# Performance work log

Hardware: AMD Instinct MI355X
Metric: run time of the kernel (lower is better)

Reference implementation:

```python
import jax, jax.numpy as jnp
import numpy as np

B, M, D, H, FF = 2, 2048, 1024, 16, 2624
DH = D // H  # 64, power of 2 as required by the kernel
EPS = 1e-5
THETA = 10000.0


def setup_inputs() -> dict:
    key = jax.random.key(0)
    ks = jax.random.split(key, 12)
    hidden_states = jax.random.normal(ks[0], (B, M, D), dtype=jnp.float32)
    # padding mask: 1=valid, 0=pad; vary valid lengths per batch element
    lengths = jnp.array([M, 3 * M // 4], dtype=jnp.int32)
    attention_mask = (jnp.arange(M)[None, :] < lengths[:, None]).astype(jnp.int32)
    s = 0.02
    return {
        "hidden_states": hidden_states,
        "attention_mask": attention_mask,
        "ln1_w": jnp.ones((D,), jnp.float32),
        "ln1_b": jnp.zeros((D,), jnp.float32),
        "wqkv_w": s * jax.random.normal(ks[1], (3 * D, D), jnp.float32),
        "wqkv_b": jnp.zeros((3 * D,), jnp.float32),
        "wo_w": s * jax.random.normal(ks[2], (D, D), jnp.float32),
        "ln2_w": jnp.ones((D,), jnp.float32),
        "ln2_b": jnp.zeros((D,), jnp.float32),
        "wi_w": s * jax.random.normal(ks[3], (2 * FF, D), jnp.float32),
        "wo_mlp_w": s * jax.random.normal(ks[4], (D, FF), jnp.float32),
    }


def _layernorm(x, w, b):
    mu = jnp.mean(x, axis=-1, keepdims=True)
    var = jnp.mean(jnp.square(x - mu), axis=-1, keepdims=True)
    return (x - mu) * jax.lax.rsqrt(var + EPS) * w + b


def _rope(q, k):
    # q,k: [B,H,M,DH]; half-split RoPE (q1' = q1*c - q2*s; q2' = q1*s + q2*c)
    half = DH // 2
    inv_freq = 1.0 / (THETA ** (jnp.arange(0, DH, 2, dtype=jnp.float32) / DH))  # [half]
    freqs = jnp.arange(M, dtype=jnp.float32)[:, None] * inv_freq[None, :]      # [M, half]
    c = jnp.cos(freqs)[None, None]  # [1,1,M,half]
    s = jnp.sin(freqs)[None, None]
    q1, q2 = q[..., :half], q[..., half:]
    k1, k2 = k[..., :half], k[..., half:]
    q = jnp.concatenate([q1 * c - q2 * s, q1 * s + q2 * c], axis=-1)
    k = jnp.concatenate([k1 * c - k2 * s, k1 * s + k2 * c], axis=-1)
    return q, k


def reference(hidden_states, attention_mask, ln1_w, ln1_b, wqkv_w, wqkv_b,
              wo_w, ln2_w, ln2_b, wi_w, wo_mlp_w):
    x = hidden_states
    xn = _layernorm(x, ln1_w, ln1_b)
    qkv = (xn @ wqkv_w.T + wqkv_b).reshape(B, M, 3, H, DH)
    q, k, v = [jnp.transpose(qkv[:, :, i], (0, 2, 1, 3)) for i in range(3)]  # [B,H,M,DH]
    q, k = _rope(q, k)
    scale = 1.0 / np.sqrt(DH)
    scores = jnp.einsum("bhmd,bhnd->bhmn", q, k) * scale
    keep = (attention_mask > 0)[:, None, None, :]  # [B,1,1,M] key-padding mask
    scores = jnp.where(keep, scores, -jnp.inf)
    attn = jax.nn.softmax(scores, axis=-1)
    o = jnp.einsum("bhmn,bhnd->bhmd", attn, v)
    attn_out = jnp.transpose(o, (0, 2, 1, 3)).reshape(B, M, D)
    x = x + attn_out @ wo_w.T
    # ModernBERT GeGLU MLP
    h = _layernorm(x, ln2_w, ln2_b)
    g = h @ wi_w.T
    inp, gate = g[..., :FF], g[..., FF:]
    x = x + (jax.nn.gelu(inp, approximate=False) * gate) @ wo_mlp_w.T
    return x
```

## Files before the change

### kernel.cpp

```cpp
#include <hip/hip_runtime.h>
#include <hip/hip_bf16.h>
#include <math.h>

#define BB 2
#define MM 2048
#define DD 1024
#define HH 16
#define DHH 64
#define FF_ 2624
#define FFP 2688
#define TT (BB*MM)

typedef unsigned short u16;
typedef __attribute__((ext_vector_type(4))) unsigned short ushort4v;
typedef __attribute__((ext_vector_type(8))) short short8;
typedef __attribute__((ext_vector_type(4))) float floatx4;

#define SCALE2 0.18033688011112043f

__device__ __forceinline__ u16 f2bf(float f) {
    __hip_bfloat16 h = __float2bfloat16(f);
    return *(u16*)&h;
}
__device__ __forceinline__ float bf2f(u16 u) {
    __hip_bfloat16 h; *(u16*)&h = u;
    return __bfloat162float(h);
}
__device__ __forceinline__ float gelu_exact(float x) {
    return 0.5f * x * (1.0f + erff(x * 0.70710678118654752f));
}
__device__ __forceinline__ void gload_lds16(const void* g, void* l) {
    __builtin_amdgcn_global_load_lds(
        (const __attribute__((address_space(1))) unsigned int*)g,
        (__attribute__((address_space(3))) unsigned int*)l, 16, 0, 0);
}

__device__ __forceinline__ int xcd_swizzle(int id, int nb) {
    if (nb & 7) return id;
    return (id & 7) * (nb >> 3) + (id >> 3);
}

__global__ void cvt_all(const float* __restrict__ wqkv, const float* __restrict__ wo,
                        const float* __restrict__ wi, const float* __restrict__ womlp,
                        u16* __restrict__ dqkv, u16* __restrict__ dwo,
                        u16* __restrict__ dinp, u16* __restrict__ dgate,
                        u16* __restrict__ dmlp, float2* __restrict__ tab) {
    int bid = blockIdx.x, tid = threadIdx.x;
    if (bid < 3072) {
        int i = (bid * 256 + tid) * 4;
        float4 v = *(const float4*)(wqkv + i);
        ushort4v o = {f2bf(v.x), f2bf(v.y), f2bf(v.z), f2bf(v.w)};
        *(ushort4v*)(dqkv + i) = o;
    } else if (bid < 4096) {
        int i = ((bid - 3072) * 256 + tid) * 4;
        float4 v = *(const float4*)(wo + i);
        ushort4v o = {f2bf(v.x), f2bf(v.y), f2bf(v.z), f2bf(v.w)};
        *(ushort4v*)(dwo + i) = o;
    } else if (bid < 4096 + 2 * FFP) {
        int seg = (bid - 4096) / FFP;
        int row = (bid - 4096) % FFP;
        u16* dst = seg ? dgate : dinp;
        const float* src = wi + (size_t)(seg ? FF_ : 0) * DD;
        int c = tid * 4;
        ushort4v o = {0, 0, 0, 0};
        if (row < FF_) {
            float4 v = *(const float4*)(src + (size_t)row * DD + c);
            o.x = f2bf(v.x); o.y = f2bf(v.y); o.z = f2bf(v.z); o.w = f2bf(v.w);
        }
        *(ushort4v*)(dst + (size_t)row * DD + c) = o;
    } else if (bid < 4096 + 2 * FFP + 1024) {
        int row = bid - 4096 - 2 * FFP;
        for (int c = tid * 4; c < FFP; c += 1024) {
            ushort4v o = {0, 0, 0, 0};
            if (c < FF_) {
                float4 v = *(const float4*)(womlp + (size_t)row * FF_ + c);
                o.x = f2bf(v.x); o.y = f2bf(v.y); o.z = f2bf(v.z); o.w = f2bf(v.w);
            }
            *(ushort4v*)(dmlp + (size_t)row * FFP + c) = o;
        }
    } else {
        int bq = bid - (4096 + 2 * FFP + 1024);
        int base = bq * 1024;
        for (int idx = tid; idx < 1024; idx += 256) {
            int e = base + idx;
            int mi = e >> 5, i = e & 31;
            float fr = (float)mi * powf(10000.0f, -(float)i / 32.0f);
            tab[e] = make_float2(cosf(fr), sinf(fr));
        }
    }
}

__global__ void ln_kernel(const float* __restrict__ x, const float* __restrict__ w,
                          const float* __restrict__ b, u16* __restrict__ out) {
    int row = blockIdx.x;
    int tid = threadIdx.x;
    const float4 v = ((const float4*)(x + (size_t)row * DD))[tid];
    float s  = v.x + v.y + v.z + v.w;
    float ss = v.x*v.x + v.y*v.y + v.z*v.z + v.w*v.w;
    #pragma unroll
    for (int o = 32; o > 0; o >>= 1) { s += __shfl_down(s, o); ss += __shfl_down(ss, o); }
    __shared__ float sbuf[4], ssbuf[4];
    int wid = tid >> 6;
    if ((tid & 63) == 0) { sbuf[wid] = s; ssbuf[wid] = ss; }
    __syncthreads();
    float st  = sbuf[0] + sbuf[1] + sbuf[2] + sbuf[3];
    float sst = ssbuf[0] + ssbuf[1] + ssbuf[2] + ssbuf[3];
    float mean = st * (1.0f / DD);
    float var  = sst * (1.0f / DD) - mean * mean;
    float rstd = rsqrtf(var + 1e-5f);
    const float4 wv = ((const float4*)w)[tid];
    const float4 bv = ((const float4*)b)[tid];
    ushort4v o;
    o.x = f2bf((v.x - mean) * rstd * wv.x + bv.x);
    o.y = f2bf((v.y - mean) * rstd * wv.y + bv.y);
    o.z = f2bf((v.z - mean) * rstd * wv.z + bv.z);
    o.w = f2bf((v.w - mean) * rstd * wv.w + bv.w);
    ((ushort4v*)(out + (size_t)row * DD))[tid] = o;
}


template<int MODE, bool OUT_BF16>
__global__ __launch_bounds__(256)
void mfma_gemm(const u16* __restrict__ A, const u16* __restrict__ W,
               const float* __restrict__ bias, const void* __restrict__ add,
               void* __restrict__ Cout, int N, int K) {
    __shared__ u16 As[2][128 * 32];
    __shared__ u16 Bs[2][128 * 32];
    int tid = threadIdx.x;
    int w = tid >> 6, lane = tid & 63;
    int q = lane >> 4, m = lane & 15;

    int nbx = gridDim.x;
    int id = xcd_swizzle(blockIdx.y * nbx + blockIdx.x, nbx * gridDim.y);
    int bx = id % nbx, by = id / nbx;
    int row0 = by * 128, col0 = bx * 128;
    int wm = (w >> 1) * 64, wn = (w & 1) * 64;

    floatx4 acc[4][4];
    #pragma unroll
    for (int i = 0; i < 4; i++)
        #pragma unroll
        for (int j = 0; j < 4; j++)
            acc[i][j] = (floatx4){0.f, 0.f, 0.f, 0.f};

    int lrow = lane >> 2;
    int lcg  = (lane & 3) ^ ((lrow >> 1) & 3);
    const u16* Ag = A + (size_t)(row0 + w * 32 + lrow) * K + lcg * 8;
    const u16* Bg = W + (size_t)(col0 + w * 32 + lrow) * K + lcg * 8;
    int NT = K >> 5;
    int slot8 = (q ^ ((m >> 1) & 3)) * 8;

    gload_lds16(Ag,                    &As[0][(w * 32) * 32]);
    gload_lds16(Ag + (size_t)16 * K,   &As[0][(w * 32 + 16) * 32]);
    gload_lds16(Bg,                    &Bs[0][(w * 32) * 32]);
    gload_lds16(Bg + (size_t)16 * K,   &Bs[0][(w * 32 + 16) * 32]);
    __syncthreads();

    for (int t = 0; t < NT; ++t) {
        int cur = t & 1;
        if (t + 1 < NT) {
            const u16* Aq = Ag + (size_t)(t + 1) * 32;
            const u16* Bq = Bg + (size_t)(t + 1) * 32;
            gload_lds16(Aq,                  &As[cur ^ 1][(w * 32) * 32]);
            gload_lds16(Aq + (size_t)16 * K, &As[cur ^ 1][(w * 32 + 16) * 32]);
            gload_lds16(Bq,                  &Bs[cur ^ 1][(w * 32) * 32]);
            gload_lds16(Bq + (size_t)16 * K, &Bs[cur ^ 1][(w * 32 + 16) * 32]);
        }
        short8 af[4], bf[4];
        #pragma unroll
        for (int f = 0; f < 4; f++) {
            af[f] = *(const short8*)&As[cur][(wm + f * 16 + m) * 32 + slot8];
            bf[f] = *(const short8*)&Bs[cur][(wn + f * 16 + m) * 32 + slot8];
        }
        __builtin_amdgcn_s_setprio(1);
        #pragma unroll
        for (int mf = 0; mf < 4; mf++)
            #pragma unroll
            for (int nf = 0; nf < 4; nf++)
                acc[mf][nf] = __builtin_amdgcn_mfma_f32_16x16x32_bf16(
                    af[mf], bf[nf], acc[mf][nf], 0, 0, 0);
        __builtin_amdgcn_s_setprio(0);
        if (t + 1 < NT) __syncthreads();
    }

    #pragma unroll
    for (int nf = 0; nf < 4; nf++) {
        int col = col0 + wn + nf * 16 + m;
        float bv = 0.f;
        if (MODE == 0 && bias) bv = bias[col];
        #pragma unroll
        for (int mf = 0; mf < 4; mf++) {
            #pragma unroll
            for (int r = 0; r < 4; r++) {
                int row = row0 + wm + mf * 16 + q * 4 + r;
                size_t idx = (size_t)row * N + col;
                float vacc = acc[mf][nf][r] + bv;
                if (MODE == 1) vacc += ((const float*)add)[idx];
                if (OUT_BF16) ((u16*)Cout)[idx] = f2bf(vacc);
                else          ((float*)Cout)[idx] = vacc;
            }
        }
    }
}

__global__ __launch_bounds__(256)
void mfma_gemm_qkv(const u16* __restrict__ A, const u16* __restrict__ W,
                   const float* __restrict__ bias, const float2* __restrict__ tab,
                   u16* __restrict__ qb, u16* __restrict__ kb, u16* __restrict__ vtb) {
    __shared__ u16 As[2][128 * 32];
    __shared__ u16 Bs[2][128 * 32];
    int tid = threadIdx.x;
    int w = tid >> 6, lane = tid & 63;
    int q = lane >> 4, m = lane & 15;

    int nbx = gridDim.x;
    int id = xcd_swizzle(blockIdx.y * nbx + blockIdx.x, nbx * gridDim.y);
    int bx = id % nbx, by = id / nbx;
    int row0 = by * 128, col0 = bx * 128;
    int wm = (w >> 1) * 64, wn = (w & 1) * 64;

    floatx4 acc[4][4];
    #pragma unroll
    for (int i = 0; i < 4; i++)
        #pragma unroll
        for (int j = 0; j < 4; j++)
            acc[i][j] = (floatx4){0.f, 0.f, 0.f, 0.f};

    int lrow = lane >> 2;
    int lcg  = (lane & 3) ^ ((lrow >> 1) & 3);
    const u16* Ag = A + (size_t)(row0 + w * 32 + lrow) * DD + lcg * 8;
    const u16* Bg = W + (size_t)(col0 + w * 32 + lrow) * DD + lcg * 8;
    const int NT = DD >> 5;
    int slot8 = (q ^ ((m >> 1) & 3)) * 8;

    gload_lds16(Ag,                     &As[0][(w * 32) * 32]);
    gload_lds16(Ag + (size_t)16 * DD,   &As[0][(w * 32 + 16) * 32]);
    gload_lds16(Bg,                     &Bs[0][(w * 32) * 32]);
    gload_lds16(Bg + (size_t)16 * DD,   &Bs[0][(w * 32 + 16) * 32]);
    __syncthreads();

    for (int t = 0; t < NT; ++t) {
        int cur = t & 1;
        if (t + 1 < NT) {
            const u16* Aq = Ag + (size_t)(t + 1) * 32;
            const u16* Bq = Bg + (size_t)(t + 1) * 32;
            gload_lds16(Aq,                   &As[cur ^ 1][(w * 32) * 32]);
            gload_lds16(Aq + (size_t)16 * DD, &As[cur ^ 1][(w * 32 + 16) * 32]);
            gload_lds16(Bq,                   &Bs[cur ^ 1][(w * 32) * 32]);
            gload_lds16(Bq + (size_t)16 * DD, &Bs[cur ^ 1][(w * 32 + 16) * 32]);
        }
        short8 af[4], bf[4];
        #pragma unroll
        for (int f = 0; f < 4; f++) {
            af[f] = *(const short8*)&As[cur][(wm + f * 16 + m) * 32 + slot8];
            bf[f] = *(const short8*)&Bs[cur][(wn + f * 16 + m) * 32 + slot8];
        }
        __builtin_amdgcn_s_setprio(1);
        #pragma unroll
        for (int mf = 0; mf < 4; mf++)
            #pragma unroll
            for (int nf = 0; nf < 4; nf++)
                acc[mf][nf] = __builtin_amdgcn_mfma_f32_16x16x32_bf16(
                    af[mf], bf[nf], acc[mf][nf], 0, 0, 0);
        __builtin_amdgcn_s_setprio(0);
        if (t + 1 < NT) __syncthreads();
    }

    int wcol = col0 + wn;
    int seg  = wcol >> 6;
    int b    = row0 >> 11;
    int mi0  = (row0 & 2047) + wm;

    float b0[4];
    #pragma unroll
    for (int nf = 0; nf < 4; nf++) b0[nf] = bias[wcol + nf * 16 + m];

    if (seg < 32) {
        int hq = seg & 15;
        u16* dst = (seg < 16 ? qb : kb) + (size_t)(b * HH + hq) * MM * DHH;
        #pragma unroll
        for (int mf = 0; mf < 4; mf++) {
            #pragma unroll
            for (int r = 0; r < 4; r++) {
                int mi = mi0 + mf * 16 + q * 4 + r;
                float2 cs0 = tab[mi * 32 + m];
                float2 cs1 = tab[mi * 32 + 16 + m];
                float a0 = acc[mf][0][r] + b0[0];
                float a1 = acc[mf][1][r] + b0[1];
                float a2 = acc[mf][2][r] + b0[2];
                float a3 = acc[mf][3][r] + b0[3];
                size_t base = (size_t)mi * DHH;
                dst[base + m]      = f2bf(a0 * cs0.x - a2 * cs0.y);
                dst[base + 32 + m] = f2bf(a0 * cs0.y + a2 * cs0.x);
                dst[base + 16 + m] = f2bf(a1 * cs1.x - a3 * cs1.y);
                dst[base + 48 + m] = f2bf(a1 * cs1.y + a3 * cs1.x);
            }
        }
    } else {
        int hv = seg & 15;
        u16* dst = vtb + (size_t)(b * HH + hv) * DHH * MM;
        #pragma unroll
        for (int nf = 0; nf < 4; nf++) {
            int d = nf * 16 + m;
            #pragma unroll
            for (int mf = 0; mf < 4; mf++) {
                int mi = mi0 + mf * 16 + q * 4;
                ushort4v o;
                o.x = f2bf(acc[mf][nf][0] + b0[nf]);
                o.y = f2bf(acc[mf][nf][1] + b0[nf]);
                o.z = f2bf(acc[mf][nf][2] + b0[nf]);
                o.w = f2bf(acc[mf][nf][3] + b0[nf]);
                *(ushort4v*)(dst + (size_t)d * MM + mi) = o;
            }
        }
    }
}

__global__ __launch_bounds__(256, 2)
void mfma_gemm_glu(const u16* __restrict__ A, const u16* __restrict__ W1,
                   const u16* __restrict__ W2, u16* __restrict__ Cout) {
    __shared__ u16 As [2][128 * 32];
    __shared__ u16 B1s[2][128 * 32];
    __shared__ u16 B2s[2][128 * 32];
    int tid = threadIdx.x;
    int w = tid >> 6, lane = tid & 63;
    int q = lane >> 4, m = lane & 15;

    int nbx = gridDim.x;
    int id = xcd_swizzle(blockIdx.y * nbx + blockIdx.x, nbx * gridDim.y);
    int bx = id % nbx, by = id / nbx;
    int row0 = by * 128, col0 = bx * 128;
    int wm = (w >> 1) * 64, wn = (w & 1) * 64;

    floatx4 acc1[4][4], acc2[4][4];
    #pragma unroll
    for (int i = 0; i < 4; i++)
        #pragma unroll
        for (int j = 0; j < 4; j++) {
            acc1[i][j] = (floatx4){0.f, 0.f, 0.f, 0.f};
            acc2[i][j] = (floatx4){0.f, 0.f, 0.f, 0.f};
        }

    int lrow = lane >> 2;
    int lcg  = (lane & 3) ^ ((lrow >> 1) & 3);
    const u16* Ag  = A  + (size_t)(row0 + w * 32 + lrow) * DD + lcg * 8;
    const u16* B1g = W1 + (size_t)(col0 + w * 32 + lrow) * DD + lcg * 8;
    const u16* B2g = W2 + (size_t)(col0 + w * 32 + lrow) * DD + lcg * 8;
    const int NT = DD >> 5;
    int slot8 = (q ^ ((m >> 1) & 3)) * 8;

    gload_lds16(Ag,                    &As [0][(w * 32) * 32]);
    gload_lds16(Ag  + (size_t)16 * DD, &As [0][(w * 32 + 16) * 32]);
    gload_lds16(B1g,                   &B1s[0][(w * 32) * 32]);
    gload_lds16(B1g + (size_t)16 * DD, &B1s[0][(w * 32 + 16) * 32]);
    gload_lds16(B2g,                   &B2s[0][(w * 32) * 32]);
    gload_lds16(B2g + (size_t)16 * DD, &B2s[0][(w * 32 + 16) * 32]);
    __syncthreads();

    for (int t = 0; t < NT; ++t) {
        int cur = t & 1;
        if (t + 1 < NT) {
            const u16* Aq  = Ag  + (size_t)(t + 1) * 32;
            const u16* B1q = B1g + (size_t)(t + 1) * 32;
            const u16* B2q = B2g + (size_t)(t + 1) * 32;
            gload_lds16(Aq,                    &As [cur ^ 1][(w * 32) * 32]);
            gload_lds16(Aq  + (size_t)16 * DD, &As [cur ^ 1][(w * 32 + 16) * 32]);
            gload_lds16(B1q,                   &B1s[cur ^ 1][(w * 32) * 32]);
            gload_lds16(B1q + (size_t)16 * DD, &B1s[cur ^ 1][(w * 32 + 16) * 32]);
            gload_lds16(B2q,                   &B2s[cur ^ 1][(w * 32) * 32]);
            gload_lds16(B2q + (size_t)16 * DD, &B2s[cur ^ 1][(w * 32 + 16) * 32]);
        }
        short8 af[4], b1f[4], b2f[4];
        #pragma unroll
        for (int f = 0; f < 4; f++) {
            af[f]  = *(const short8*)&As [cur][(wm + f * 16 + m) * 32 + slot8];
            b1f[f] = *(const short8*)&B1s[cur][(wn + f * 16 + m) * 32 + slot8];
            b2f[f] = *(const short8*)&B2s[cur][(wn + f * 16 + m) * 32 + slot8];
        }
        __builtin_amdgcn_s_setprio(1);
        #pragma unroll
        for (int mf = 0; mf < 4; mf++)
            #pragma unroll
            for (int nf = 0; nf < 4; nf++) {
                acc1[mf][nf] = __builtin_amdgcn_mfma_f32_16x16x32_bf16(
                    af[mf], b1f[nf], acc1[mf][nf], 0, 0, 0);
                acc2[mf][nf] = __builtin_amdgcn_mfma_f32_16x16x32_bf16(
                    af[mf], b2f[nf], acc2[mf][nf], 0, 0, 0);
            }
        __builtin_amdgcn_s_setprio(0);
        if (t + 1 < NT) __syncthreads();
    }

    #pragma unroll
    for (int nf = 0; nf < 4; nf++) {
        int col = col0 + wn + nf * 16 + m;
        #pragma unroll
        for (int mf = 0; mf < 4; mf++) {
            #pragma unroll
            for (int r = 0; r < 4; r++) {
                int row = row0 + wm + mf * 16 + q * 4 + r;
                Cout[(size_t)row * FFP + col] =
                    f2bf(gelu_exact(acc1[mf][nf][r]) * acc2[mf][nf][r]);
            }
        }
    }
}

__global__ __launch_bounds__(256, 2)
void flash_attn_mfma(const u16* __restrict__ q, const u16* __restrict__ k,
                     const u16* __restrict__ vt, const int* __restrict__ mask,
                     u16* __restrict__ out) {
    __shared__ __align__(16) u16 Ks[64 * 64];
    __shared__ __align__(16) u16 Vt[64 * 64];
    __shared__ __align__(16) u16 QP[128 * 64];

    int tid = threadIdx.x;
    int w = tid >> 6, lane = tid & 63;
    int quad = lane >> 4, m = lane & 15;
    int mt = blockIdx.x, h = blockIdx.y, b = blockIdx.z;
    int m0 = mt * 128;
    size_t bh = (size_t)(b * HH + h);
    const u16* qb  = q  + (bh * MM + m0) * DHH;
    const u16* kb  = k  + bh * MM * DHH;
    const u16* vtb = vt + bh * DHH * MM;

    int lrow = lane >> 3, lcg = (lane & 7) ^ lrow;

    {
        const u16* Qg = qb + (size_t)(w * 32 + lrow) * DHH + lcg * 8;
        u16* Ql = &QP[(w * 32) * 64];
        #pragma unroll
        for (int t = 0; t < 4; t++)
            gload_lds16(Qg + (size_t)(t * 8) * DHH, Ql + t * 8 * 64);
    }
    __syncthreads();

    short8 qf[2][2];
    #pragma unroll
    for (int mf = 0; mf < 2; mf++)
        #pragma unroll
        for (int ks = 0; ks < 2; ks++) {
            int slot = (ks * 4 + quad) ^ (m & 7);
            qf[mf][ks] = *(const short8*)&QP[(w * 32 + mf * 16 + m) * 64 + slot * 8];
        }

    floatx4 O[2][4];
    #pragma unroll
    for (int mf = 0; mf < 2; mf++)
        #pragma unroll
        for (int df = 0; df < 4; df++)
            O[mf][df] = (floatx4){0.f, 0.f, 0.f, 0.f};
    float lsum[2][4] = {};

    u16* Pw = &QP[(w * 32) * 64];

    for (int n0 = 0; n0 < MM; n0 += 64) {
        if (mask[b * MM + n0] == 0) break;
        __syncthreads();

        {
            const u16* Kg = kb + (size_t)(n0 + w * 16 + lrow) * DHH + lcg * 8;
            u16* Kl = &Ks[(w * 16) * 64];
            #pragma unroll
            for (int t = 0; t < 2; t++)
                gload_lds16(Kg + (size_t)(t * 8) * DHH, Kl + t * 8 * 64);
            const u16* Vg = vtb + (size_t)(w * 16 + lrow) * MM + n0 + lcg * 8;
            u16* Vl = &Vt[(w * 16) * 64];
            #pragma unroll
            for (int t = 0; t < 2; t++)
                gload_lds16(Vg + (size_t)(t * 8) * MM, Vl + t * 8 * 64);
        }
        __syncthreads();

        floatx4 S[2][4];
        #pragma unroll
        for (int mf = 0; mf < 2; mf++)
            #pragma unroll
            for (int nf = 0; nf < 4; nf++)
                S[mf][nf] = (floatx4){0.f, 0.f, 0.f, 0.f};
        #pragma unroll
        for (int ks = 0; ks < 2; ks++) {
            short8 kf[4];
            #pragma unroll
            for (int nf = 0; nf < 4; nf++) {
                int slot = (ks * 4 + quad) ^ (m & 7);
                kf[nf] = *(const short8*)&Ks[(nf * 16 + m) * 64 + slot * 8];
            }
            #pragma unroll
            for (int mf = 0; mf < 2; mf++)
                #pragma unroll
                for (int nf = 0; nf < 4; nf++)
                    S[mf][nf] = __builtin_amdgcn_mfma_f32_16x16x32_bf16(
                        qf[mf][ks], kf[nf], S[mf][nf], 0, 0, 0);
        }

        #pragma unroll
        for (int mf = 0; mf < 2; mf++)
            #pragma unroll
            for (int r = 0; r < 4; r++) {
                float s0 = exp2f(S[mf][0][r] * SCALE2);
                float s1 = exp2f(S[mf][1][r] * SCALE2);
                float s2 = exp2f(S[mf][2][r] * SCALE2);
                float s3 = exp2f(S[mf][3][r] * SCALE2);
                S[mf][0][r] = s0; S[mf][1][r] = s1; S[mf][2][r] = s2; S[mf][3][r] = s3;
                lsum[mf][r] += (s0 + s1) + (s2 + s3);
            }

        #pragma unroll
        for (int mf = 0; mf < 2; mf++)
            #pragma unroll
            for (int nf = 0; nf < 4; nf++)
                #pragma unroll
                for (int r = 0; r < 4; r++) {
                    int prow = mf * 16 + quad * 4 + r;
                    int pcol = nf * 16 + m;
                    int slot = (pcol >> 3) ^ (prow & 7);
                    Pw[prow * 64 + slot * 8 + (pcol & 7)] = f2bf(S[mf][nf][r]);
                }

        #pragma unroll
        for (int ks = 0; ks < 2; ks++) {
            short8 pf[2], vf[4];
            #pragma unroll
            for (int mf = 0; mf < 2; mf++) {
                int slot = (ks * 4 + quad) ^ (m & 7);
                pf[mf] = *(const short8*)&Pw[(mf * 16 + m) * 64 + slot * 8];
            }
            #pragma unroll
            for (int df = 0; df < 4; df++) {
                int d = df * 16 + m;
                int slot = (ks * 4 + quad) ^ (d & 7);
                vf[df] = *(const short8*)&Vt[d * 64 + slot * 8];
            }
            #pragma unroll
            for (int mf = 0; mf < 2; mf++)
                #pragma unroll
                for (int df = 0; df < 4; df++)
                    O[mf][df] = __builtin_amdgcn_mfma_f32_16x16x32_bf16(
                        pf[mf], vf[df], O[mf][df], 0, 0, 0);
        }
    }

    #pragma unroll
    for (int mf = 0; mf < 2; mf++) {
        float inv[4];
        #pragma unroll
        for (int r = 0; r < 4; r++) {
            float s = lsum[mf][r];
            #pragma unroll
            for (int o = 1; o < 16; o <<= 1) s += __shfl_xor(s, o);
            inv[r] = 1.0f / s;
        }
        #pragma unroll
        for (int df = 0; df < 4; df++) {
            int d = df * 16 + m;
            #pragma unroll
            for (int r = 0; r < 4; r++) {
                int row = m0 + w * 32 + mf * 16 + quad * 4 + r;
                out[((size_t)(b * MM) + row) * DD + h * DHH + d] =
                    f2bf(O[mf][df][r] * inv[r]);
            }
        }
    }
}

extern "C" void kernel_launch(void* const* d_in, const int* in_sizes, int n_in,
                              void* d_out, int out_size, void* d_ws, size_t ws_size,
                              hipStream_t stream) {
    const float* hidden   = (const float*)d_in[0];
    const int*   mask     = (const int*)d_in[1];
    const float* ln1_w    = (const float*)d_in[2];
    const float* ln1_b    = (const float*)d_in[3];
    const float* wqkv_w   = (const float*)d_in[4];
    const float* wqkv_b   = (const float*)d_in[5];
    const float* wo_w     = (const float*)d_in[6];
    const float* ln2_w    = (const float*)d_in[7];
    const float* ln2_b    = (const float*)d_in[8];
    const float* wi_w     = (const float*)d_in[9];
    const float* wo_mlp_w = (const float*)d_in[10];
    float* out = (float*)d_out;

    char* ws = (char*)d_ws;
    u16* wqkv_bf  = (u16*)(ws);
    u16* wo_bf    = (u16*)(ws + 6291456);
    u16* wi_inp   = (u16*)(ws + 8388608);
    u16* wi_gate  = (u16*)(ws + 13893632);
    u16* womlp_bf = (u16*)(ws + 19398656);
    u16* xn       = (u16*)(ws + 24903680);
    float2* rtab  = (float2*)(ws + 33292288);
    u16* qb       = (u16*)(ws + 58458112);
    u16* kb       = (u16*)(ws + 66846720);
    u16* vtb      = (u16*)(ws + 75235328);
    u16* attn_out = (u16*)(ws + 83623936);
    u16* hb       = (u16*)(ws + 92012544);
    u16* act      = (u16*)(ws + 58458112);

    cvt_all<<<4096 + 2 * FFP + 1024 + 64, 256, 0, stream>>>(
        wqkv_w, wo_w, wi_w, wo_mlp_w, wqkv_bf, wo_bf, wi_inp, wi_gate, womlp_bf, rtab);
    ln_kernel<<<TT, 256, 0, stream>>>(hidden, ln1_w, ln1_b, xn);
    mfma_gemm_qkv<<<dim3(3 * DD / 128, TT / 128), 256, 0, stream>>>(
        xn, wqkv_bf, wqkv_b, rtab, qb, kb, vtb);
    flash_attn_mfma<<<dim3(MM / 128, HH, BB), 256, 0, stream>>>(qb, kb, vtb, mask, attn_out);
    mfma_gemm<1, false><<<dim3(DD / 128, TT / 128), 256, 0, stream>>>(
        attn_out, wo_bf, nullptr, hidden, out, DD, DD);
    ln_kernel<<<TT, 256, 0, stream>>>(out, ln2_w, ln2_b, hb);
    mfma_gemm_glu<<<dim3(FFP / 128, TT / 128), 256, 0, stream>>>(
        hb, wi_inp, wi_gate, act);
    mfma_gemm<1, false><<<dim3(DD / 128, TT / 128), 256, 0, stream>>>(
        act, womlp_bf, nullptr, out, out, DD, FFP);
}
```

Measured before the change: 411.6 us.

## Shrink GEMM tiles to 128x64 and use explicit vmcnt waits with raw barriers

```diff
diff --git a/kernel.cpp b/kernel.cpp
--- a/kernel.cpp
+++ b/kernel.cpp
@@ -17,6 +17,9 @@
 typedef __attribute__((ext_vector_type(4))) float floatx4;
 
 #define SCALE2 0.18033688011112043f
+
+#define WAITVM(N) asm volatile("s_waitcnt vmcnt(" #N ")" ::: "memory")
+#define CFENCE()  asm volatile("" ::: "memory")
 
 __device__ __forceinline__ u16 f2bf(float f) {
     __hip_bfloat16 h = __float2bfloat16(f);
@@ -120,12 +123,12 @@
 
 
 template<int MODE, bool OUT_BF16>
-__global__ __launch_bounds__(256)
-void mfma_gemm(const u16* __restrict__ A, const u16* __restrict__ W,
-               const float* __restrict__ bias, const void* __restrict__ add,
-               void* __restrict__ Cout, int N, int K) {
+__global__ __launch_bounds__(256, 4)
+void mfma_gemm64(const u16* __restrict__ A, const u16* __restrict__ W,
+                 const float* __restrict__ bias, const void* __restrict__ add,
+                 void* __restrict__ Cout, int N, int K) {
     __shared__ u16 As[2][128 * 32];
-    __shared__ u16 Bs[2][128 * 32];
+    __shared__ u16 Bs[2][64 * 32];
     int tid = threadIdx.x;
     int w = tid >> 6, lane = tid & 63;
     int q = lane >> 4, m = lane & 15;
@@ -133,28 +136,26 @@
     int nbx = gridDim.x;
     int id = xcd_swizzle(blockIdx.y * nbx + blockIdx.x, nbx * gridDim.y);
     int bx = id % nbx, by = id / nbx;
-    int row0 = by * 128, col0 = bx * 128;
-    int wm = (w >> 1) * 64, wn = (w & 1) * 64;
-
-    floatx4 acc[4][4];
+    int row0 = by * 128, col0 = bx * 64;
+    int wm = (w >> 1) * 64, wn = (w & 1) * 32;
+
+    floatx4 acc[4][2];
     #pragma unroll
     for (int i = 0; i < 4; i++)
         #pragma unroll
-        for (int j = 0; j < 4; j++)
+        for (int j = 0; j < 2; j++)
             acc[i][j] = (floatx4){0.f, 0.f, 0.f, 0.f};
 
     int lrow = lane >> 2;
     int lcg  = (lane & 3) ^ ((lrow >> 1) & 3);
     const u16* Ag = A + (size_t)(row0 + w * 32 + lrow) * K + lcg * 8;
-    const u16* Bg = W + (size_t)(col0 + w * 32 + lrow) * K + lcg * 8;
+    const u16* Bg = W + (size_t)(col0 + w * 16 + lrow) * K + lcg * 8;
     int NT = K >> 5;
     int slot8 = (q ^ ((m >> 1) & 3)) * 8;
 
-    gload_lds16(Ag,                    &As[0][(w * 32) * 32]);
-    gload_lds16(Ag + (size_t)16 * K,   &As[0][(w * 32 + 16) * 32]);
-    gload_lds16(Bg,                    &Bs[0][(w * 32) * 32]);
-    gload_lds16(Bg + (size_t)16 * K,   &Bs[0][(w * 32 + 16) * 32]);
-    __syncthreads();
+    gload_lds16(Ag,                  &As[0][(w * 32) * 32]);
+    gload_lds16(Ag + (size_t)16 * K, &As[0][(w * 32 + 16) * 32]);
+    gload_lds16(Bg,                  &Bs[0][(w * 16) * 32]);
 
     for (int t = 0; t < NT; ++t) {
         int cur = t & 1;
@@ -163,28 +164,36 @@
             const u16* Bq = Bg + (size_t)(t + 1) * 32;
             gload_lds16(Aq,                  &As[cur ^ 1][(w * 32) * 32]);
             gload_lds16(Aq + (size_t)16 * K, &As[cur ^ 1][(w * 32 + 16) * 32]);
-            gload_lds16(Bq,                  &Bs[cur ^ 1][(w * 32) * 32]);
-            gload_lds16(Bq + (size_t)16 * K, &Bs[cur ^ 1][(w * 32 + 16) * 32]);
-        }
-        short8 af[4], bf[4];
-        #pragma unroll
-        for (int f = 0; f < 4; f++) {
+            gload_lds16(Bq,                  &Bs[cur ^ 1][(w * 16) * 32]);
+            WAITVM(3);
+        } else {
+            WAITVM(0);
+        }
+        __builtin_amdgcn_s_barrier();
+        CFENCE();
+        short8 af[4], bf[2];
+        #pragma unroll
+        for (int f = 0; f < 4; f++)
             af[f] = *(const short8*)&As[cur][(wm + f * 16 + m) * 32 + slot8];
+        #pragma unroll
+        for (int f = 0; f < 2; f++)
             bf[f] = *(const short8*)&Bs[cur][(wn + f * 16 + m) * 32 + slot8];
-        }
         __builtin_amdgcn_s_setprio(1);
         #pragma unroll
         for (int mf = 0; mf < 4; mf++)
             #pragma unroll
-            for (int nf = 0; nf < 4; nf++)
+            for (int nf = 0; nf < 2; nf++)
                 acc[mf][nf] = __builtin_amdgcn_mfma_f32_16x16x32_bf16(
                     af[mf], bf[nf], acc[mf][nf], 0, 0, 0);
         __builtin_amdgcn_s_setprio(0);
-        if (t + 1 < NT) __syncthreads();
-    }
-
-    #pragma unroll
-    for (int nf = 0; nf < 4; nf++) {
+        if (t + 1 < NT) {
+            __builtin_amdgcn_s_barrier();
+            CFENCE();
+        }
+    }
+
+    #pragma unroll
+    for (int nf = 0; nf < 2; nf++) {
         int col = col0 + wn + nf * 16 + m;
         float bv = 0.f;
         if (MODE == 0 && bias) bv = bias[col];
@@ -203,12 +212,12 @@
     }
 }
 
-__global__ __launch_bounds__(256)
+__global__ __launch_bounds__(256, 4)
 void mfma_gemm_qkv(const u16* __restrict__ A, const u16* __restrict__ W,
                    const float* __restrict__ bias, const float2* __restrict__ tab,
                    u16* __restrict__ qb, u16* __restrict__ kb, u16* __restrict__ vtb) {
     __shared__ u16 As[2][128 * 32];
-    __shared__ u16 Bs[2][128 * 32];
+    __shared__ u16 Bs[2][64 * 32];
     int tid = threadIdx.x;
     int w = tid >> 6, lane = tid & 63;
     int q = lane >> 4, m = lane & 15;
@@ -216,12 +225,12 @@
     int nbx = gridDim.x;
     int id = xcd_swizzle(blockIdx.y * nbx + blockIdx.x, nbx * gridDim.y);
     int bx = id % nbx, by = id / nbx;
-    int row0 = by * 128, col0 = bx * 128;
-    int wm = (w >> 1) * 64, wn = (w & 1) * 64;
-
-    floatx4 acc[4][4];
-    #pragma unroll
-    for (int i = 0; i < 4; i++)
+    int row0 = by * 128, col0 = bx * 64;
+    int wm = w * 32;
+
+    floatx4 acc[2][4];
+    #pragma unroll
+    for (int i = 0; i < 2; i++)
         #pragma unroll
         for (int j = 0; j < 4; j++)
             acc[i][j] = (floatx4){0.f, 0.f, 0.f, 0.f};
@@ -229,15 +238,13 @@
     int lrow = lane >> 2;
     int lcg  = (lane & 3) ^ ((lrow >> 1) & 3);
     const u16* Ag = A + (size_t)(row0 + w * 32 + lrow) * DD + lcg * 8;
-    const u16* Bg = W + (size_t)(col0 + w * 32 + lrow) * DD + lcg * 8;
+    const u16* Bg = W + (size_t)(col0 + w * 16 + lrow) * DD + lcg * 8;
     const int NT = DD >> 5;
     int slot8 = (q ^ ((m >> 1) & 3)) * 8;
 
-    gload_lds16(Ag,                     &As[0][(w * 32) * 32]);
-    gload_lds16(Ag + (size_t)16 * DD,   &As[0][(w * 32 + 16) * 32]);
-    gload_lds16(Bg,                     &Bs[0][(w * 32) * 32]);
-    gload_lds16(Bg + (size_t)16 * DD,   &Bs[0][(w * 32 + 16) * 32]);
-    __syncthreads();
+    gload_lds16(Ag,                   &As[0][(w * 32) * 32]);
+    gload_lds16(Ag + (size_t)16 * DD, &As[0][(w * 32 + 16) * 32]);
+    gload_lds16(Bg,                   &Bs[0][(w * 16) * 32]);
 
     for (int t = 0; t < NT; ++t) {
         int cur = t & 1;
@@ -246,40 +253,47 @@
             const u16* Bq = Bg + (size_t)(t + 1) * 32;
             gload_lds16(Aq,                   &As[cur ^ 1][(w * 32) * 32]);
             gload_lds16(Aq + (size_t)16 * DD, &As[cur ^ 1][(w * 32 + 16) * 32]);
-            gload_lds16(Bq,                   &Bs[cur ^ 1][(w * 32) * 32]);
-            gload_lds16(Bq + (size_t)16 * DD, &Bs[cur ^ 1][(w * 32 + 16) * 32]);
-        }
-        short8 af[4], bf[4];
-        #pragma unroll
-        for (int f = 0; f < 4; f++) {
+            gload_lds16(Bq,                   &Bs[cur ^ 1][(w * 16) * 32]);
+            WAITVM(3);
+        } else {
+            WAITVM(0);
+        }
+        __builtin_amdgcn_s_barrier();
+        CFENCE();
+        short8 af[2], bf[4];
+        #pragma unroll
+        for (int f = 0; f < 2; f++)
             af[f] = *(const short8*)&As[cur][(wm + f * 16 + m) * 32 + slot8];
-            bf[f] = *(const short8*)&Bs[cur][(wn + f * 16 + m) * 32 + slot8];
-        }
+        #pragma unroll
+        for (int f = 0; f < 4; f++)
+            bf[f] = *(const short8*)&Bs[cur][(f * 16 + m) * 32 + slot8];
         __builtin_amdgcn_s_setprio(1);
         #pragma unroll
-        for (int mf = 0; mf < 4; mf++)
+        for (int mf = 0; mf < 2; mf++)
             #pragma unroll
             for (int nf = 0; nf < 4; nf++)
                 acc[mf][nf] = __builtin_amdgcn_mfma_f32_16x16x32_bf16(
                     af[mf], bf[nf], acc[mf][nf], 0, 0, 0);
         __builtin_amdgcn_s_setprio(0);
-        if (t + 1 < NT) __syncthreads();
-    }
-
-    int wcol = col0 + wn;
-    int seg  = wcol >> 6;
-    int b    = row0 >> 11;
-    int mi0  = (row0 & 2047) + wm;
+        if (t + 1 < NT) {
+            __builtin_amdgcn_s_barrier();
+            CFENCE();
+        }
+    }
+
+    int seg = col0 >> 6;
+    int b   = row0 >> 11;
+    int mi0 = (row0 & 2047) + wm;
 
     float b0[4];
     #pragma unroll
-    for (int nf = 0; nf < 4; nf++) b0[nf] = bias[wcol + nf * 16 + m];
+    for (int nf = 0; nf < 4; nf++) b0[nf] = bias[col0 + nf * 16 + m];
 
     if (seg < 32) {
         int hq = seg & 15;
         u16* dst = (seg < 16 ? qb : kb) + (size_t)(b * HH + hq) * MM * DHH;
         #pragma unroll
-        for (int mf = 0; mf < 4; mf++) {
+        for (int mf = 0; mf < 2; mf++) {
             #pragma unroll
             for (int r = 0; r < 4; r++) {
                 int mi = mi0 + mf * 16 + q * 4 + r;
@@ -303,7 +317,7 @@
         for (int nf = 0; nf < 4; nf++) {
             int d = nf * 16 + m;
             #pragma unroll
-            for (int mf = 0; mf < 4; mf++) {
+            for (int mf = 0; mf < 2; mf++) {
                 int mi = mi0 + mf * 16 + q * 4;
                 ushort4v o;
                 o.x = f2bf(acc[mf][nf][0] + b0[nf]);
@@ -316,12 +330,12 @@
     }
 }
 
-__global__ __launch_bounds__(256, 2)
+__global__ __launch_bounds__(256, 4)
 void mfma_gemm_glu(const u16* __restrict__ A, const u16* __restrict__ W1,
                    const u16* __restrict__ W2, u16* __restrict__ Cout) {
     __shared__ u16 As [2][128 * 32];
-    __shared__ u16 B1s[2][128 * 32];
-    __shared__ u16 B2s[2][128 * 32];
+    __shared__ u16 B1s[2][64 * 32];
+    __shared__ u16 B2s[2][64 * 32];
     int tid = threadIdx.x;
     int w = tid >> 6, lane = tid & 63;
     int q = lane >> 4, m = lane & 15;
@@ -329,14 +343,14 @@
     int nbx = gridDim.x;
     int id = xcd_swizzle(blockIdx.y * nbx + blockIdx.x, nbx * gridDim.y);
     int bx = id % nbx, by = id / nbx;
-    int row0 = by * 128, col0 = bx * 128;
-    int wm = (w >> 1) * 64, wn = (w & 1) * 64;
-
-    floatx4 acc1[4][4], acc2[4][4];
+    int row0 = by * 128, col0 = bx * 64;
+    int wm = (w >> 1) * 64, wn = (w & 1) * 32;
+
+    floatx4 acc1[4][2], acc2[4][2];
     #pragma unroll
     for (int i = 0; i < 4; i++)
         #pragma unroll
-        for (int j = 0; j < 4; j++) {
+        for (int j = 0; j < 2; j++) {
             acc1[i][j] = (floatx4){0.f, 0.f, 0.f, 0.f};
             acc2[i][j] = (floatx4){0.f, 0.f, 0.f, 0.f};
         }
@@ -344,18 +358,15 @@
     int lrow = lane >> 2;
     int lcg  = (lane & 3) ^ ((lrow >> 1) & 3);
     const u16* Ag  = A  + (size_t)(row0 + w * 32 + lrow) * DD + lcg * 8;
-    const u16* B1g = W1 + (size_t)(col0 + w * 32 + lrow) * DD + lcg * 8;
-    const u16* B2g = W2 + (size_t)(col0 + w * 32 + lrow) * DD + lcg * 8;
+    const u16* B1g = W1 + (size_t)(col0 + w * 16 + lrow) * DD + lcg * 8;
+    const u16* B2g = W2 + (size_t)(col0 + w * 16 + lrow) * DD + lcg * 8;
     const int NT = DD >> 5;
     int slot8 = (q ^ ((m >> 1) & 3)) * 8;
 
     gload_lds16(Ag,                    &As [0][(w * 32) * 32]);
     gload_lds16(Ag  + (size_t)16 * DD, &As [0][(w * 32 + 16) * 32]);
-    gload_lds16(B1g,                   &B1s[0][(w * 32) * 32]);
-    gload_lds16(B1g + (size_t)16 * DD, &B1s[0][(w * 32 + 16) * 32]);
-    gload_lds16(B2g,                   &B2s[0][(w * 32) * 32]);
-    gload_lds16(B2g + (size_t)16 * DD, &B2s[0][(w * 32 + 16) * 32]);
-    __syncthreads();
+    gload_lds16(B1g,                   &B1s[0][(w * 16) * 32]);
+    gload_lds16(B2g,                   &B2s[0][(w * 16) * 32]);
 
     for (int t = 0; t < NT; ++t) {
         int cur = t & 1;
@@ -365,15 +376,20 @@
             const u16* B2q = B2g + (size_t)(t + 1) * 32;
             gload_lds16(Aq,                    &As [cur ^ 1][(w * 32) * 32]);
             gload_lds16(Aq  + (size_t)16 * DD, &As [cur ^ 1][(w * 32 + 16) * 32]);
-            gload_lds16(B1q,                   &B1s[cur ^ 1][(w * 32) * 32]);
-            gload_lds16(B1q + (size_t)16 * DD, &B1s[cur ^ 1][(w * 32 + 16) * 32]);
-            gload_lds16(B2q,                   &B2s[cur ^ 1][(w * 32) * 32]);
-            gload_lds16(B2q + (size_t)16 * DD, &B2s[cur ^ 1][(w * 32 + 16) * 32]);
-        }
-        short8 af[4], b1f[4], b2f[4];
-        #pragma unroll
-        for (int f = 0; f < 4; f++) {
-            af[f]  = *(const short8*)&As [cur][(wm + f * 16 + m) * 32 + slot8];
+            gload_lds16(B1q,                   &B1s[cur ^ 1][(w * 16) * 32]);
+            gload_lds16(B2q,                   &B2s[cur ^ 1][(w * 16) * 32]);
+            WAITVM(4);
+        } else {
+            WAITVM(0);
+        }
+        __builtin_amdgcn_s_barrier();
+        CFENCE();
+        short8 af[4], b1f[2], b2f[2];
+        #pragma unroll
+        for (int f = 0; f < 4; f++)
+            af[f] = *(const short8*)&As[cur][(wm + f * 16 + m) * 32 + slot8];
+        #pragma unroll
+        for (int f = 0; f < 2; f++) {
             b1f[f] = *(const short8*)&B1s[cur][(wn + f * 16 + m) * 32 + slot8];
             b2f[f] = *(const short8*)&B2s[cur][(wn + f * 16 + m) * 32 + slot8];
         }
@@ -381,18 +397,21 @@
         #pragma unroll
         for (int mf = 0; mf < 4; mf++)
             #pragma unroll
-            for (int nf = 0; nf < 4; nf++) {
+            for (int nf = 0; nf < 2; nf++) {
                 acc1[mf][nf] = __builtin_amdgcn_mfma_f32_16x16x32_bf16(
                     af[mf], b1f[nf], acc1[mf][nf], 0, 0, 0);
                 acc2[mf][nf] = __builtin_amdgcn_mfma_f32_16x16x32_bf16(
                     af[mf], b2f[nf], acc2[mf][nf], 0, 0, 0);
             }
         __builtin_amdgcn_s_setprio(0);
-        if (t + 1 < NT) __syncthreads();
-    }
-
-    #pragma unroll
-    for (int nf = 0; nf < 4; nf++) {
+        if (t + 1 < NT) {
+            __builtin_amdgcn_s_barrier();
+            CFENCE();
+        }
+    }
+
+    #pragma unroll
+    for (int nf = 0; nf < 2; nf++) {
         int col = col0 + wn + nf * 16 + m;
         #pragma unroll
         for (int mf = 0; mf < 4; mf++) {
@@ -598,14 +617,14 @@
     cvt_all<<<4096 + 2 * FFP + 1024 + 64, 256, 0, stream>>>(
         wqkv_w, wo_w, wi_w, wo_mlp_w, wqkv_bf, wo_bf, wi_inp, wi_gate, womlp_bf, rtab);
     ln_kernel<<<TT, 256, 0, stream>>>(hidden, ln1_w, ln1_b, xn);
-    mfma_gemm_qkv<<<dim3(3 * DD / 128, TT / 128), 256, 0, stream>>>(
+    mfma_gemm_qkv<<<dim3(3 * DD / 64, TT / 128), 256, 0, stream>>>(
         xn, wqkv_bf, wqkv_b, rtab, qb, kb, vtb);
     flash_attn_mfma<<<dim3(MM / 128, HH, BB), 256, 0, stream>>>(qb, kb, vtb, mask, attn_out);
-    mfma_gemm<1, false><<<dim3(DD / 128, TT / 128), 256, 0, stream>>>(
+    mfma_gemm64<1, false><<<dim3(DD / 64, TT / 128), 256, 0, stream>>>(
         attn_out, wo_bf, nullptr, hidden, out, DD, DD);
     ln_kernel<<<TT, 256, 0, stream>>>(out, ln2_w, ln2_b, hb);
-    mfma_gemm_glu<<<dim3(FFP / 128, TT / 128), 256, 0, stream>>>(
+    mfma_gemm_glu<<<dim3(FFP / 64, TT / 128), 256, 0, stream>>>(
         hb, wi_inp, wi_gate, act);
-    mfma_gemm<1, false><<<dim3(DD / 128, TT / 128), 256, 0, stream>>>(
+    mfma_gemm64<1, false><<<dim3(DD / 64, TT / 128), 256, 0, stream>>>(
         act, womlp_bf, nullptr, out, out, DD, FFP);
 }
```

Result: faster. 377.5 us (-8.3%).
